# Performance work log

Hardware: AMD Instinct MI355X
Metric: run time of the kernel (lower is better)

## Reference

```python
import jax, jax.numpy as jnp
import numpy as np

D_MODEL = 1024
H = 16
D = D_MODEL // H  # 64 per-head dim
B, T = 2, 2048


def setup_inputs() -> dict:
    key = jax.random.key(0)
    ks = jax.random.split(key, 5)
    scale = 1.0 / np.sqrt(D_MODEL)
    x = jax.random.normal(ks[0], (B, T, D_MODEL), dtype=jnp.float32)
    Wqkv = jax.random.normal(ks[1], (D_MODEL, 3 * D_MODEL), dtype=jnp.float32) * scale
    bqkv = jnp.zeros((3 * D_MODEL,), dtype=jnp.float32)
    Wproj = jax.random.normal(ks[2], (D_MODEL, D_MODEL), dtype=jnp.float32) * scale
    bproj = jnp.zeros((D_MODEL,), dtype=jnp.float32)
    return {"x": x, "Wqkv": Wqkv, "bqkv": bqkv, "Wproj": Wproj, "bproj": bproj}


def reference(x, Wqkv, bqkv, Wproj, bproj):
    b, t, d_model = x.shape
    h, d = H, D
    qkv = x @ Wqkv + bqkv  # [b, t, 3*d_model]
    q, k, v = jnp.split(qkv, 3, axis=-1)
    # [b, t, d_model] -> [b, h, t, d]
    q = q.reshape(b, t, h, d).transpose(0, 2, 1, 3)
    k = k.reshape(b, t, h, d).transpose(0, 2, 1, 3)
    v = v.reshape(b, t, h, d).transpose(0, 2, 1, 3)
    att = jnp.einsum('bhqd,bhkd->bhqk', q, k) / jnp.sqrt(jnp.float32(d))
    causal = jnp.tril(jnp.ones((t, t), dtype=bool))  # [t, t]
    att = jnp.where(causal[None, None, :, :], att, -jnp.inf)
    att = jax.nn.softmax(att, axis=-1)
    # dropout in eval mode -> identity (deterministic reference)
    out = jnp.einsum('bhqk,bhkd->bhqd', att, v)  # [b, h, t, d]
    out = out.transpose(0, 2, 1, 3).reshape(b, t, d_model)
    out = out @ Wproj + bproj
    return out
```

## Files before the change

### kernel.cpp

```cpp
#include <hip/hip_runtime.h>
#include <cstddef>

typedef __bf16 bf16x8 __attribute__((ext_vector_type(8)));
typedef float  f32x4  __attribute__((ext_vector_type(4)));

__device__ __forceinline__ float bf2f(unsigned short s) {
    return __uint_as_float(((unsigned int)s) << 16);
}
__device__ __forceinline__ unsigned short f2bf(float x) {
    unsigned int u = __float_as_uint(x);
    unsigned int r = u + 0x7fffu + ((u >> 16) & 1u);
    return (unsigned short)(r >> 16);
}

__device__ __forceinline__ void async_load16(const void* g, void* l) {
    __builtin_amdgcn_global_load_lds(
        (const __attribute__((address_space(1))) unsigned int*)g,
        (__attribute__((address_space(3))) unsigned int*)l,
        16, 0, 0);
}

__global__ __launch_bounds__(256) void prep_kernel(
    const void* __restrict__ x, const void* __restrict__ Wqkv,
    const void* __restrict__ Wproj,
    unsigned short* __restrict__ xb, unsigned short* __restrict__ WqkvT,
    unsigned short* __restrict__ WprojT, int* __restrict__ flagp)
{
    __shared__ unsigned short T[64][72];
    __shared__ int cnt;
    const int tid = threadIdx.x;
    const int bid = blockIdx.x;

    if (tid == 0) cnt = 0;
    __syncthreads();
    {
        unsigned short u = ((const unsigned short*)x)[tid << 1];
        int e = (u >> 7) & 0xFF;
        int wild = ((e >= 0x90) || (e >= 1 && e <= 0x48)) ? 1 : 0;
        unsigned long long ball = __ballot(wild);
        if ((tid & 63) == 0) atomicAdd(&cnt, (int)__popcll(ball));
    }
    __syncthreads();
    const bool f32 = (cnt > 64);
    if (bid == 0 && tid == 0) *flagp = f32 ? 1 : 0;

    if (bid < 2048) {
        const size_t off = ((size_t)bid * 256 + tid) * 8;
        if (f32) {
            const float* s = (const float*)x + off;
            float4 a = *(const float4*)s;
            float4 b = *(const float4*)(s + 4);
            uint4 o;
            o.x = (unsigned)f2bf(a.x) | ((unsigned)f2bf(a.y) << 16);
            o.y = (unsigned)f2bf(a.z) | ((unsigned)f2bf(a.w) << 16);
            o.z = (unsigned)f2bf(b.x) | ((unsigned)f2bf(b.y) << 16);
            o.w = (unsigned)f2bf(b.z) | ((unsigned)f2bf(b.w) << 16);
            *(uint4*)(xb + off) = o;
        } else {
            *(uint4*)(xb + off) = *(const uint4*)((const unsigned short*)x + off);
        }
        return;
    }

    const void* src; unsigned short* dst; int C, bx, by;
    if (bid < 2048 + 768) {
        const int t2 = bid - 2048;
        src = Wqkv; dst = WqkvT; C = 3072;
        bx = t2 % 48; by = t2 / 48;
    } else {
        const int t2 = bid - 2816;
        src = Wproj; dst = WprojT; C = 1024;
        bx = t2 % 16; by = t2 / 16;
    }
    const int R = 1024;
    const int c0 = bx * 64, r0 = by * 64;
    const int r  = tid >> 2, cl = (tid & 3) << 4;

    unsigned short v[16];
    if (f32) {
        const float* s = (const float*)src + (size_t)(r0 + r) * C + c0 + cl;
        #pragma unroll
        for (int q = 0; q < 4; ++q) {
            float4 a = *(const float4*)(s + q * 4);
            v[q * 4 + 0] = f2bf(a.x); v[q * 4 + 1] = f2bf(a.y);
            v[q * 4 + 2] = f2bf(a.z); v[q * 4 + 3] = f2bf(a.w);
        }
    } else {
        const unsigned short* s = (const unsigned short*)src + (size_t)(r0 + r) * C + c0 + cl;
        uint4 a = *(const uint4*)s;
        uint4 b = *(const uint4*)(s + 8);
        unsigned int w[8] = {a.x, a.y, a.z, a.w, b.x, b.y, b.z, b.w};
        #pragma unroll
        for (int q = 0; q < 8; ++q) {
            v[q * 2]     = (unsigned short)(w[q] & 0xffffu);
            v[q * 2 + 1] = (unsigned short)(w[q] >> 16);
        }
    }
    #pragma unroll
    for (int c = 0; c < 16; ++c) T[cl + c][r] = v[c];
    __syncthreads();

    const int c = tid >> 2, rl = (tid & 3) << 4;
    uint4 o0 = *(const uint4*)&T[c][rl];
    uint4 o1 = *(const uint4*)&T[c][rl + 8];
    unsigned short* dp = dst + (size_t)(c0 + c) * R + r0 + rl;
    *(uint4*)dp       = o0;
    *(uint4*)(dp + 8) = o1;
}

__device__ __forceinline__ void bt_mainloop(
    const unsigned short* __restrict__ A,
    const unsigned short* __restrict__ BT,
    int K, int m0, int n0,
    unsigned short* As, unsigned short* Bs,
    f32x4 (&acc)[4][4])
{
    const int tid  = threadIdx.x;
    const int wave = tid >> 6;
    const int lane = tid & 63;
    const int mrow = lane & 15;
    const int quad = lane >> 4;
    const int wr = wave >> 1, wc = wave & 1;
    const int srow = tid >> 2;
    const int scol = (tid & 3) << 3;

    const unsigned short* ga  = A  + (size_t)(m0 + srow) * K + scol;
    const unsigned short* ga2 = ga + (size_t)64 * K;
    const unsigned short* gb  = BT + (size_t)(n0 + srow) * K + scol;
    const unsigned short* gb2 = gb + (size_t)64 * K;
    unsigned short* lA  = As + wave * 512;
    unsigned short* lA2 = As + 2048 + wave * 512;
    unsigned short* lB  = Bs + wave * 512;
    unsigned short* lB2 = Bs + 2048 + wave * 512;

    for (int k0 = 0; k0 < K; k0 += 32) {
        async_load16(ga,  lA);
        async_load16(ga2, lA2);
        async_load16(gb,  lB);
        async_load16(gb2, lB2);
        ga += 32; ga2 += 32; gb += 32; gb2 += 32;
        __syncthreads();

        bf16x8 afr[4], bfr[4];
        #pragma unroll
        for (int mt = 0; mt < 4; ++mt)
            afr[mt] = *(const bf16x8*)(As + (wr * 64 + mt * 16 + mrow) * 32 + quad * 8);
        #pragma unroll
        for (int nt = 0; nt < 4; ++nt)
            bfr[nt] = *(const bf16x8*)(Bs + (wc * 64 + nt * 16 + mrow) * 32 + quad * 8);
        #pragma unroll
        for (int mt = 0; mt < 4; ++mt) {
            #pragma unroll
            for (int nt = 0; nt < 4; ++nt)
                acc[mt][nt] = __builtin_amdgcn_mfma_f32_16x16x32_bf16(
                    afr[mt], bfr[nt], acc[mt][nt], 0, 0, 0);
        }
        __syncthreads();
    }
}

__global__ __launch_bounds__(256) void gemm_qkv_bt(
    const int* __restrict__ flag,
    const unsigned short* __restrict__ A,
    const unsigned short* __restrict__ BT,
    const void* __restrict__ bias,
    unsigned short* __restrict__ Qb, unsigned short* __restrict__ Kb,
    unsigned short* __restrict__ VbT)
{
    __shared__ unsigned short As[128 * 32];
    __shared__ unsigned short Bs[128 * 32];
    const int m0 = blockIdx.y * 128, n0 = blockIdx.x * 128;

    f32x4 acc[4][4];
    #pragma unroll
    for (int mt = 0; mt < 4; ++mt)
        #pragma unroll
        for (int nt = 0; nt < 4; ++nt)
            { acc[mt][nt][0]=0.f; acc[mt][nt][1]=0.f; acc[mt][nt][2]=0.f; acc[mt][nt][3]=0.f; }

    bt_mainloop(A, BT, 1024, m0, n0, As, Bs, acc);

    const int tid  = threadIdx.x;
    const int wave = tid >> 6;
    const int lane = tid & 63;
    const int mrow = lane & 15;
    const int quad = lane >> 4;
    const int wr = wave >> 1, wc = wave & 1;
    const bool f32b = (*flag != 0);

    #pragma unroll
    for (int nt = 0; nt < 4; ++nt) {
        const int n = n0 + wc * 64 + nt * 16 + mrow;
        const float bv = f32b ? ((const float*)bias)[n]
                              : bf2f(((const unsigned short*)bias)[n]);
        const int sel = n >> 10;
        const int h   = (n & 1023) >> 6;
        const int d   = n & 63;
        const float sc = (sel == 0) ? 0.125f : 1.0f;
        #pragma unroll
        for (int mt = 0; mt < 4; ++mt) {
            #pragma unroll
            for (int r = 0; r < 4; ++r) {
                const int m  = m0 + wr * 64 + mt * 16 + quad * 4 + r;
                const int bb = m >> 11;
                const int t  = m & 2047;
                const unsigned short ov = f2bf((acc[mt][nt][r] + bv) * sc);
                const int bhh = bb * 16 + h;
                if (sel == 0)      Qb [(((size_t)bhh * 2048 + t) << 6) + d] = ov;
                else if (sel == 1) Kb [(((size_t)bhh * 2048 + t) << 6) + d] = ov;
                else               VbT[((((size_t)bhh << 6) + d) << 11) + t] = ov;
            }
        }
    }
}

__global__ __launch_bounds__(256) void gemm_proj_n64(
    const int* __restrict__ flag,
    const unsigned short* __restrict__ A,
    const unsigned short* __restrict__ BT,
    const void* __restrict__ bias, void* __restrict__ Out)
{
    __shared__ unsigned short As[128 * 32];
    __shared__ unsigned short Bs[64 * 32];
    const int K = 1024;
    const int m0 = blockIdx.y * 128, n0 = blockIdx.x * 64;

    const int tid  = threadIdx.x;
    const int wave = tid >> 6;
    const int lane = tid & 63;
    const int mrow = lane & 15;
    const int quad = lane >> 4;
    const int wr = wave >> 1, wc = wave & 1;
    const int srow = tid >> 2;
    const int scol = (tid & 3) << 3;

    f32x4 acc[4][2];
    #pragma unroll
    for (int mt = 0; mt < 4; ++mt)
        #pragma unroll
        for (int nt = 0; nt < 2; ++nt)
            { acc[mt][nt][0]=0.f; acc[mt][nt][1]=0.f; acc[mt][nt][2]=0.f; acc[mt][nt][3]=0.f; }

    const unsigned short* ga  = A  + (size_t)(m0 + srow) * K + scol;
    const unsigned short* ga2 = ga + (size_t)64 * K;
    const unsigned short* gb  = BT + (size_t)(n0 + srow) * K + scol;
    unsigned short* lA  = As + wave * 512;
    unsigned short* lA2 = As + 2048 + wave * 512;
    unsigned short* lB  = Bs + wave * 512;

    for (int k0 = 0; k0 < K; k0 += 32) {
        async_load16(ga,  lA);
        async_load16(ga2, lA2);
        async_load16(gb,  lB);
        ga += 32; ga2 += 32; gb += 32;
        __syncthreads();

        bf16x8 afr[4], bfr[2];
        #pragma unroll
        for (int mt = 0; mt < 4; ++mt)
            afr[mt] = *(const bf16x8*)(As + (wr * 64 + mt * 16 + mrow) * 32 + quad * 8);
        #pragma unroll
        for (int nt = 0; nt < 2; ++nt)
            bfr[nt] = *(const bf16x8*)(Bs + (wc * 32 + nt * 16 + mrow) * 32 + quad * 8);
        #pragma unroll
        for (int mt = 0; mt < 4; ++mt) {
            #pragma unroll
            for (int nt = 0; nt < 2; ++nt)
                acc[mt][nt] = __builtin_amdgcn_mfma_f32_16x16x32_bf16(
                    afr[mt], bfr[nt], acc[mt][nt], 0, 0, 0);
        }
        __syncthreads();
    }

    const bool f32b = (*flag != 0);
    #pragma unroll
    for (int nt = 0; nt < 2; ++nt) {
        const int n = n0 + wc * 32 + nt * 16 + mrow;
        const float bv = f32b ? ((const float*)bias)[n]
                              : bf2f(((const unsigned short*)bias)[n]);
        #pragma unroll
        for (int mt = 0; mt < 4; ++mt) {
            #pragma unroll
            for (int r = 0; r < 4; ++r) {
                const int m = m0 + wr * 64 + mt * 16 + quad * 4 + r;
                const float val = acc[mt][nt][r] + bv;
                if (f32b) ((float*)Out)[(size_t)m * 1024 + n] = val;
                else      ((unsigned short*)Out)[(size_t)m * 1024 + n] = f2bf(val);
            }
        }
    }
}

__global__ __launch_bounds__(256) void attn_kernel(
    const unsigned short* __restrict__ Qb,
    const unsigned short* __restrict__ Kb,
    const unsigned short* __restrict__ VbT,
    unsigned short* __restrict__ Attn)
{
    __shared__ unsigned short Ks2[2][2][64 * 32];
    __shared__ unsigned short Vs2[2][2][64 * 32];
    __shared__ unsigned short Ps[64 * 64];

    const int tid  = threadIdx.x;
    const int wave = tid >> 6;
    const int lane = tid & 63;
    const int mrow = lane & 15;
    const int quad = lane >> 4;

    const int blk  = blockIdx.x;
    const int xcd  = blk & 7;
    const int j    = blk >> 3;
    const int s    = j >> 5;
    const int w    = j & 31;
    const int t8   = w >> 2;
    const int bh   = (xcd << 2) | (w & 3);
    const int qblk = (s == 0) ? 31 - t8 : (s == 1) ? 23 - t8
                   : (s == 2) ? 8 + t8   : t8;
    const int q0   = qblk << 6;
    const int nr   = qblk + 1;
    const int b    = bh >> 4, h = bh & 15;

    const int lc    = tid & 63;
    const int sc_   = lc ^ ((lc >> 3) & 7);
    const int grow  = wave * 16 + (sc_ >> 2);
    const int gcol8 = (sc_ & 3) << 3;
    const int ldst  = tid * 8;

    const int swzro = ((mrow * 4 + quad) ^ ((mrow >> 1) & 7)) << 3;

    const unsigned short* Qbase = Qb  + ((size_t)bh << 17);
    const unsigned short* Kbase = Kb  + ((size_t)bh << 17);
    const unsigned short* Vtb   = VbT + ((size_t)bh << 17);

    bf16x8 ones;
    #pragma unroll
    for (int e = 0; e < 8; ++e) ones[e] = (__bf16)1.0f;

    bf16x8 aq[2];
    {
        const unsigned short* qp = Qbase + (size_t)(q0 + wave * 16 + mrow) * 64 + quad * 8;
        aq[0] = *(const bf16x8*)qp;
        aq[1] = *(const bf16x8*)(qp + 32);
    }

    f32x4 Oa[4];
    #pragma unroll
    for (int dt = 0; dt < 4; ++dt) { Oa[dt][0]=0.f; Oa[dt][1]=0.f; Oa[dt][2]=0.f; Oa[dt][3]=0.f; }
    f32x4 la; la[0]=0.f; la[1]=0.f; la[2]=0.f; la[3]=0.f;

    #pragma unroll
    for (int h2 = 0; h2 < 2; ++h2)
        async_load16(Kbase + (size_t)grow * 64 + h2 * 32 + gcol8,
                     &Ks2[0][h2][ldst]);
    #pragma unroll
    for (int j2 = 0; j2 < 2; ++j2)
        async_load16(Vtb + ((size_t)grow << 11) + j2 * 32 + gcol8,
                     &Vs2[0][j2][ldst]);

    for (int rr = 0; rr < nr; ++rr) {
        __syncthreads();

        if (rr + 1 < nr) {
            const int nt0 = (rr + 1) << 6;
            const int nb  = (rr + 1) & 1;
            #pragma unroll
            for (int h2 = 0; h2 < 2; ++h2)
                async_load16(Kbase + (size_t)(nt0 + grow) * 64 + h2 * 32 + gcol8,
                             &Ks2[nb][h2][ldst]);
            #pragma unroll
            for (int j2 = 0; j2 < 2; ++j2)
                async_load16(Vtb + ((size_t)grow << 11) + nt0 + j2 * 32 + gcol8,
                             &Vs2[nb][j2][ldst]);
        }

        const int cb  = rr & 1;
        const int kt0 = rr << 6;

        f32x4 sacc[4];
        #pragma unroll
        for (int jt = 0; jt < 4; ++jt) { sacc[jt][0]=0.f; sacc[jt][1]=0.f; sacc[jt][2]=0.f; sacc[jt][3]=0.f; }
        #pragma unroll
        for (int ks = 0; ks < 2; ++ks) {
            #pragma unroll
            for (int jt = 0; jt < 4; ++jt) {
                bf16x8 bk = *(const bf16x8*)&Ks2[cb][ks][jt * 512 + swzro];
                sacc[jt] = __builtin_amdgcn_mfma_f32_16x16x32_bf16(aq[ks], bk, sacc[jt], 0, 0, 0);
            }
        }

        if (rr == nr - 1) {
            #pragma unroll
            for (int jt = 0; jt < 4; ++jt) {
                const int jg = kt0 + jt * 16 + mrow;
                #pragma unroll
                for (int r = 0; r < 4; ++r) {
                    if (jg > q0 + wave * 16 + quad * 4 + r) sacc[jt][r] = -1e30f;
                }
            }
        }

        #pragma unroll
        for (int jt = 0; jt < 4; ++jt) {
            #pragma unroll
            for (int r = 0; r < 4; ++r) {
                const float pv = __expf(sacc[jt][r] - 16.0f);
                const int row = wave * 16 + quad * 4 + r;
                const int col = jt * 16 + mrow;
                Ps[row * 64 + ((((col >> 3) ^ (row & 7)) << 3) | (col & 7))] = f2bf(pv);
            }
        }

        __threadfence_block();

        const int prow = wave * 16 + mrow;
        #pragma unroll
        for (int ks2 = 0; ks2 < 2; ++ks2) {
            bf16x8 ap = *(const bf16x8*)&Ps[prow * 64 + (((ks2 * 4 + quad) ^ (mrow & 7)) << 3)];
            la = __builtin_amdgcn_mfma_f32_16x16x32_bf16(ap, ones, la, 0, 0, 0);
            #pragma unroll
            for (int dt = 0; dt < 4; ++dt) {
                bf16x8 bv = *(const bf16x8*)&Vs2[cb][ks2][dt * 512 + swzro];
                Oa[dt] = __builtin_amdgcn_mfma_f32_16x16x32_bf16(ap, bv, Oa[dt], 0, 0, 0);
            }
        }
    }

    #pragma unroll
    for (int r = 0; r < 4; ++r) {
        const float inv = 1.0f / la[r];
        const int t = q0 + wave * 16 + quad * 4 + r;
        const size_t base = ((size_t)(b * 2048 + t)) * 1024 + h * 64;
        #pragma unroll
        for (int dt = 0; dt < 4; ++dt)
            Attn[base + dt * 16 + mrow] = f2bf(Oa[dt][r] * inv);
    }
}

extern "C" void kernel_launch(void* const* d_in, const int* in_sizes, int n_in,
                              void* d_out, int out_size, void* d_ws, size_t ws_size,
                              hipStream_t stream)
{
    const void* x     = d_in[0];
    const void* Wqkv  = d_in[1];
    const void* bqkv  = d_in[2];
    const void* Wproj = d_in[3];
    const void* bproj = d_in[4];

    int* flag = (int*)d_ws;
    unsigned short* ws = (unsigned short*)d_ws;
    unsigned short* xb     = ws + 64;
    unsigned short* shared = xb + 4194304;
    unsigned short* WqkvT  = shared;
    unsigned short* Attn   = shared;
    unsigned short* WprojT = shared + 4194304;
    unsigned short* Qb     = WprojT + 1048576;
    unsigned short* Kb     = Qb + 4194304;
    unsigned short* VbT    = Kb + 4194304;

    prep_kernel<<<3072, 256, 0, stream>>>(x, Wqkv, Wproj, xb, WqkvT, WprojT, flag);
    gemm_qkv_bt<<<dim3(24, 32), 256, 0, stream>>>(flag, xb, WqkvT, bqkv, Qb, Kb, VbT);
    attn_kernel<<<1024, 256, 0, stream>>>(Qb, Kb, VbT, Attn);
    gemm_proj_n64<<<dim3(16, 32), 256, 0, stream>>>(flag, Attn, WprojT, bproj, d_out);
}
```

Before: 187.5 us.

## Keep softmax probabilities in registers by computing transposed S and feeding P directly to MFMA

The attention kernel now computes S transposed (K as the A operand), so each lane holds four consecutive key probabilities for one query row. These are packed to bf16 and used directly as the B operand of 16x16x16 MFMAs against a re-laid-out V tile, which removes the Ps shared-memory round trip and its fence. The row-sum is computed with a ones-vector MFMA per key tile. The output store is also vectorized to 8-byte packed writes. The trade-off is twice as many smaller MFMA instructions for the PV product and a new swizzled V layout in LDS.

Result: no change. 187.0 us (-0.3%).

```diff
diff --git a/kernel.cpp b/kernel.cpp
--- a/kernel.cpp
+++ b/kernel.cpp
@@ -3,6 +3,9 @@
 
 typedef __bf16 bf16x8 __attribute__((ext_vector_type(8)));
 typedef float  f32x4  __attribute__((ext_vector_type(4)));
+typedef short  s16x4  __attribute__((ext_vector_type(4)));
+
+union U64pk { unsigned u[2]; s16x4 v; };
 
 __device__ __forceinline__ float bf2f(unsigned short s) {
     return __uint_as_float(((unsigned int)s) << 16);
@@ -11,6 +14,20 @@
     unsigned int u = __float_as_uint(x);
     unsigned int r = u + 0x7fffu + ((u >> 16) & 1u);
     return (unsigned short)(r >> 16);
+}
+
+__device__ __forceinline__ unsigned cvt_pk_bf16(float lo, float hi) {
+    unsigned r;
+    asm("v_cvt_pk_bf16_f32 %0, %1, %2" : "=v"(r) : "v"(lo), "v"(hi));
+    return r;
+}
+
+__device__ __forceinline__ unsigned pack_bf16_c(float lo, float hi) {
+    return ((unsigned)f2bf(hi) << 16) | (unsigned)f2bf(lo);
+}
+
+__device__ __forceinline__ void mfma16(f32x4& c, s16x4 a, s16x4 b) {
+    c = __builtin_amdgcn_mfma_f32_16x16x16bf16_1k(a, b, c, 0, 0, 0);
 }
 
 __device__ __forceinline__ void async_load16(const void* g, void* l) {
@@ -298,8 +315,7 @@
     unsigned short* __restrict__ Attn)
 {
     __shared__ unsigned short Ks2[2][2][64 * 32];
-    __shared__ unsigned short Vs2[2][2][64 * 32];
-    __shared__ unsigned short Ps[64 * 64];
+    __shared__ unsigned short Vs2[2][64 * 64];
 
     const int tid  = threadIdx.x;
     const int wave = tid >> 6;
@@ -326,15 +342,22 @@
     const int gcol8 = (sc_ & 3) << 3;
     const int ldst  = tid * 8;
 
+    const int vrow0 = tid >> 3;
+    const int vcol  = (((tid & 7) ^ (vrow0 & 7)) << 3);
+
     const int swzro = ((mrow * 4 + quad) ^ ((mrow >> 1) & 7)) << 3;
+
+    const int m7 = mrow & 7, qh = quad >> 1, ql = quad & 1;
+    int voff[4];
+    #pragma unroll
+    for (int jt = 0; jt < 4; ++jt)
+        voff[jt] = (((2 * jt + qh) ^ m7) << 3) + (ql << 2);
 
     const unsigned short* Qbase = Qb  + ((size_t)bh << 17);
     const unsigned short* Kbase = Kb  + ((size_t)bh << 17);
     const unsigned short* Vtb   = VbT + ((size_t)bh << 17);
 
-    bf16x8 ones;
-    #pragma unroll
-    for (int e = 0; e < 8; ++e) ones[e] = (__bf16)1.0f;
+    s16x4 ones4 = { 0x3F80, 0x3F80, 0x3F80, 0x3F80 };
 
     bf16x8 aq[2];
     {
@@ -352,10 +375,8 @@
     for (int h2 = 0; h2 < 2; ++h2)
         async_load16(Kbase + (size_t)grow * 64 + h2 * 32 + gcol8,
                      &Ks2[0][h2][ldst]);
-    #pragma unroll
-    for (int j2 = 0; j2 < 2; ++j2)
-        async_load16(Vtb + ((size_t)grow << 11) + j2 * 32 + gcol8,
-                     &Vs2[0][j2][ldst]);
+    async_load16(Vtb + (size_t)vrow0 * 2048 + vcol, &Vs2[0][tid * 8]);
+    async_load16(Vtb + (size_t)(vrow0 + 32) * 2048 + vcol, &Vs2[0][2048 + tid * 8]);
 
     for (int rr = 0; rr < nr; ++rr) {
         __syncthreads();
@@ -367,10 +388,10 @@
             for (int h2 = 0; h2 < 2; ++h2)
                 async_load16(Kbase + (size_t)(nt0 + grow) * 64 + h2 * 32 + gcol8,
                              &Ks2[nb][h2][ldst]);
-            #pragma unroll
-            for (int j2 = 0; j2 < 2; ++j2)
-                async_load16(Vtb + ((size_t)grow << 11) + nt0 + j2 * 32 + gcol8,
-                             &Vs2[nb][j2][ldst]);
+            async_load16(Vtb + (size_t)vrow0 * 2048 + nt0 + vcol,
+                         &Vs2[nb][tid * 8]);
+            async_load16(Vtb + (size_t)(vrow0 + 32) * 2048 + nt0 + vcol,
+                         &Vs2[nb][2048 + tid * 8]);
         }
 
         const int cb  = rr & 1;
@@ -384,55 +405,58 @@
             #pragma unroll
             for (int jt = 0; jt < 4; ++jt) {
                 bf16x8 bk = *(const bf16x8*)&Ks2[cb][ks][jt * 512 + swzro];
-                sacc[jt] = __builtin_amdgcn_mfma_f32_16x16x32_bf16(aq[ks], bk, sacc[jt], 0, 0, 0);
+                sacc[jt] = __builtin_amdgcn_mfma_f32_16x16x32_bf16(bk, aq[ks], sacc[jt], 0, 0, 0);
             }
         }
 
         if (rr == nr - 1) {
+            const int qg = q0 + wave * 16 + mrow;
             #pragma unroll
             for (int jt = 0; jt < 4; ++jt) {
-                const int jg = kt0 + jt * 16 + mrow;
                 #pragma unroll
                 for (int r = 0; r < 4; ++r) {
-                    if (jg > q0 + wave * 16 + quad * 4 + r) sacc[jt][r] = -1e30f;
+                    const int jg = kt0 + jt * 16 + quad * 4 + r;
+                    if (jg > qg) sacc[jt][r] = -1e30f;
                 }
             }
         }
 
+        s16x4 up[4];
         #pragma unroll
         for (int jt = 0; jt < 4; ++jt) {
-            #pragma unroll
-            for (int r = 0; r < 4; ++r) {
-                const float pv = __expf(sacc[jt][r] - 16.0f);
-                const int row = wave * 16 + quad * 4 + r;
-                const int col = jt * 16 + mrow;
-                Ps[row * 64 + ((((col >> 3) ^ (row & 7)) << 3) | (col & 7))] = f2bf(pv);
+            const float p0 = __expf(sacc[jt][0] - 16.0f);
+            const float p1 = __expf(sacc[jt][1] - 16.0f);
+            const float p2 = __expf(sacc[jt][2] - 16.0f);
+            const float p3 = __expf(sacc[jt][3] - 16.0f);
+            U64pk uu;
+            uu.u[0] = pack_bf16_c(p0, p1);
+            uu.u[1] = pack_bf16_c(p2, p3);
+            up[jt] = uu.v;
+        }
+
+        #pragma unroll
+        for (int dt = 0; dt < 4; ++dt) {
+            const int vb = (dt * 16 + mrow) << 6;
+            #pragma unroll
+            for (int jt = 0; jt < 4; ++jt) {
+                s16x4 vf = *(const s16x4*)&Vs2[cb][vb + voff[jt]];
+                mfma16(Oa[dt], vf, up[jt]);
             }
         }
-
-        __threadfence_block();
-
-        const int prow = wave * 16 + mrow;
-        #pragma unroll
-        for (int ks2 = 0; ks2 < 2; ++ks2) {
-            bf16x8 ap = *(const bf16x8*)&Ps[prow * 64 + (((ks2 * 4 + quad) ^ (mrow & 7)) << 3)];
-            la = __builtin_amdgcn_mfma_f32_16x16x32_bf16(ap, ones, la, 0, 0, 0);
-            #pragma unroll
-            for (int dt = 0; dt < 4; ++dt) {
-                bf16x8 bv = *(const bf16x8*)&Vs2[cb][ks2][dt * 512 + swzro];
-                Oa[dt] = __builtin_amdgcn_mfma_f32_16x16x32_bf16(ap, bv, Oa[dt], 0, 0, 0);
-            }
-        }
-    }
-
-    #pragma unroll
-    for (int r = 0; r < 4; ++r) {
-        const float inv = 1.0f / la[r];
-        const int t = q0 + wave * 16 + quad * 4 + r;
-        const size_t base = ((size_t)(b * 2048 + t)) * 1024 + h * 64;
-        #pragma unroll
-        for (int dt = 0; dt < 4; ++dt)
-            Attn[base + dt * 16 + mrow] = f2bf(Oa[dt][r] * inv);
+        #pragma unroll
+        for (int jt = 0; jt < 4; ++jt)
+            mfma16(la, ones4, up[jt]);
+    }
+
+    const float inv = 1.0f / la[0];
+    const int   qg  = q0 + wave * 16 + mrow;
+    const size_t base = ((size_t)(b * 2048 + qg)) * 1024 + h * 64 + quad * 4;
+    #pragma unroll
+    for (int dt = 0; dt < 4; ++dt) {
+        uint2 o;
+        o.x = cvt_pk_bf16(Oa[dt][0] * inv, Oa[dt][1] * inv);
+        o.y = cvt_pk_bf16(Oa[dt][2] * inv, Oa[dt][3] * inv);
+        *(uint2*)(Attn + base + dt * 16) = o;
     }
 }
 
```
